# Kernel tuning notes

Measured on AMD Instinct MI355X. Metric: run time of the kernel, lower is better.

The kernel has to match this reference:

```python
import jax, jax.numpy as jnp
import numpy as np

HEADS = 8
DIM_HEAD = 64


def setup_inputs() -> dict:
    key = jax.random.key(0)
    ks = jax.random.split(key, 6)
    b, n, d = 4, 2048, 512
    inner = HEADS * DIM_HEAD  # 512
    return {
        "x": jax.random.normal(ks[0], (b, n, d), dtype=jnp.float32),
        "W_v": jax.random.normal(ks[1], (d, inner), dtype=jnp.float32) * 0.02,
        "W_sigma": jax.random.normal(ks[2], (d, HEADS), dtype=jnp.float32) * 0.02,
        "b_sigma": jax.random.normal(ks[3], (HEADS,), dtype=jnp.float32) * 0.02,
        "W_out": jax.random.normal(ks[4], (inner, d), dtype=jnp.float32) * 0.02,
        "b_out": jax.random.normal(ks[5], (d,), dtype=jnp.float32) * 0.02,
    }


def reference(x, W_v, W_sigma, b_sigma, W_out, b_out):
    b, n, d = x.shape
    h, dh = HEADS, DIM_HEAD
    # |i - j| distance matrix (linspace(1,n,n) differences == arange differences)
    pos = jnp.arange(n, dtype=x.dtype)
    dist = jnp.abs(pos[:, None] - pos[None, :])  # (n, n)
    # per-query-row sigma: (b, h, n)
    sigma = jax.nn.sigmoid(jnp.einsum("bnd,dh->bhn", x, W_sigma) + b_sigma[None, :, None])
    denom = jnp.exp(sigma) + 1.0  # (b, h, n)
    # prior[b,h,i,j] = softmax_j( -|i-j| / (exp(sigma[b,h,i]) + 1) )
    prior = jax.nn.softmax(-dist[None, None, :, :] / denom[..., None], axis=-1)  # (b,h,n,n)
    v = (x @ W_v).reshape(b, n, h, dh).transpose(0, 2, 1, 3)  # (b,h,n,dh)
    out = jnp.einsum("bhij,bhjd->bhid", prior, v)  # (b,h,n,dh)
    out = out.transpose(0, 2, 1, 3).reshape(b, n, h * dh)
    return out @ W_out + b_out
```

## Files before the change

### kernel.cpp

```cpp
#include <hip/hip_runtime.h>
#include <hip/hip_bf16.h>

#define B 4
#define N 2048
#define D 512
#define H 8
#define DH 64
#define ROWS (B * N)
#define WIN 64
#define LPAD 64
#define RPAD 128
#define SEG (LPAD + N + RPAD)
#define LDV (B * SEG)

using bf16x8 = __attribute__((ext_vector_type(8))) short;
using f32x4  = __attribute__((ext_vector_type(4))) float;
using f32x16 = __attribute__((ext_vector_type(16))) float;

static __device__ __forceinline__ unsigned short f2bf(float f) {
    unsigned u = __builtin_bit_cast(unsigned, f);
    u += 0x7fffu + ((u >> 16) & 1u);
    return (unsigned short)(u >> 16);
}
static __device__ __forceinline__ unsigned pack2(float a, float b) {
    return (unsigned)f2bf(a) | ((unsigned)f2bf(b) << 16);
}

__global__ __launch_bounds__(256) void prep_fused(const float* __restrict__ x,
                                                  const float* __restrict__ Ws,
                                                  const float* __restrict__ bs,
                                                  const float* __restrict__ Wv,
                                                  const float* __restrict__ Wo,
                                                  unsigned short* __restrict__ xbf,
                                                  float* __restrict__ l2rbuf,
                                                  unsigned short* __restrict__ WvT,
                                                  unsigned short* __restrict__ WoT,
                                                  unsigned short* __restrict__ Vt) {
    __shared__ float tile[64][65];
    const int bx = blockIdx.x;

    if (bx < 2048) {
        const int wid = threadIdx.x >> 6, lane = threadIdx.x & 63;
        const int row = bx * 4 + wid;
        const float* xr = x + (size_t)row * D + lane * 8;
        const float4 a = *reinterpret_cast<const float4*>(xr);
        const float4 c = *reinterpret_cast<const float4*>(xr + 4);
        float v[8] = {a.x, a.y, a.z, a.w, c.x, c.y, c.z, c.w};

        uint4 o;
        o.x = pack2(v[0], v[1]); o.y = pack2(v[2], v[3]);
        o.z = pack2(v[4], v[5]); o.w = pack2(v[6], v[7]);
        *reinterpret_cast<uint4*>(xbf + (size_t)row * D + lane * 8) = o;

        const float4* Ws4 = reinterpret_cast<const float4*>(Ws);
        f32x4 alo = (f32x4)0.0f, ahi = (f32x4)0.0f;
#pragma unroll
        for (int j = 0; j < 8; j++) {
            const int e = lane * 8 + j;
            const float4 wl = Ws4[e * 2], wh = Ws4[e * 2 + 1];
            alo[0] += v[j] * wl.x; alo[1] += v[j] * wl.y; alo[2] += v[j] * wl.z; alo[3] += v[j] * wl.w;
            ahi[0] += v[j] * wh.x; ahi[1] += v[j] * wh.y; ahi[2] += v[j] * wh.z; ahi[3] += v[j] * wh.w;
        }
#pragma unroll
        for (int off = 1; off < 64; off <<= 1) {
#pragma unroll
            for (int c2 = 0; c2 < 4; c2++) {
                alo[c2] += __shfl_xor(alo[c2], off, 64);
                ahi[c2] += __shfl_xor(ahi[c2], off, 64);
            }
        }
        if (lane < 8) {
            const int h = lane;
            const float acc = (h < 4) ? alo[h] : ahi[h - 4];
            const float z = acc + bs[h];
            const float sig = 1.0f / (1.0f + expf(-z));
            const float s = expf(sig) + 1.0f;
            l2rbuf[(size_t)row * H + h] = -1.4426950408889634f / s;
        }
        return;
    }

    if (bx < 2176) {
        const int idx = bx - 2048;
        const bool second = idx >= 64;
        const int id2 = idx & 63;
        const float* src = second ? Wo : Wv;
        unsigned short* dst = second ? WoT : WvT;
        const int n0 = (id2 & 7) * 64, k0 = (id2 >> 3) * 64;
        const int tr = threadIdx.x >> 4, tc = threadIdx.x & 15;
#pragma unroll
        for (int it = 0; it < 4; it++) {
            const int r = it * 16 + tr;
            const float4 v = *reinterpret_cast<const float4*>(&src[(size_t)(k0 + r) * 512 + n0 + tc * 4]);
            tile[r][tc * 4 + 0] = v.x; tile[r][tc * 4 + 1] = v.y;
            tile[r][tc * 4 + 2] = v.z; tile[r][tc * 4 + 3] = v.w;
        }
        __syncthreads();
#pragma unroll
        for (int it = 0; it < 4; it++) {
            const int r = it * 16 + tr;
            ushort4 o;
            o.x = f2bf(tile[tc * 4 + 0][r]); o.y = f2bf(tile[tc * 4 + 1][r]);
            o.z = f2bf(tile[tc * 4 + 2][r]); o.w = f2bf(tile[tc * 4 + 3][r]);
            *reinterpret_cast<ushort4*>(&dst[(size_t)(n0 + r) * 512 + k0 + tc * 4]) = o;
        }
        return;
    }

    {
        const int idx = bx - 2176;
        for (int t = idx * 256 + threadIdx.x; t < 512 * 4 * 24; t += 64 * 256) {
            const int c = t % 24;
            const int bb = (t / 24) & 3;
            const int row = t / 96;
            const int col = (c < 8) ? bb * SEG + c * 8 : bb * SEG + LPAD + N + (c - 8) * 8;
            *reinterpret_cast<uint4*>(Vt + (size_t)row * LDV + col) = uint4{0, 0, 0, 0};
        }
    }
}

#define GBK 64
#define GK  512

template <int MODE>
__global__ __launch_bounds__(256) void gemm_bf16(const unsigned short* __restrict__ A,
                                                 const unsigned short* __restrict__ Bt,
                                                 const float* __restrict__ bias,
                                                 void* __restrict__ Cout,
                                                 int ldc) {
    __shared__ unsigned short As[2][64][GBK];
    __shared__ unsigned short Bs[2][64][GBK];
    const int tid = threadIdx.x;
    const int lane = tid & 63, wid = tid >> 6;
    const int wr = wid >> 1, wc = wid & 1;
    int bm, bn;
    if (MODE == 0) {
        const int xcd = blockIdx.x & 7, idx = blockIdx.x >> 3;
        bm = xcd * 16 + (idx >> 3);
        bn = idx & 7;
    } else {
        bn = blockIdx.x; bm = blockIdx.y;
    }
    const int fr = lane & 15, kg = lane >> 4;

    f32x4 acc[2][2] = {};

    const unsigned short* Ab = A + (size_t)bm * 64 * GK;
    const unsigned short* Bb = Bt + (size_t)bn * 64 * GK;
    const int r32 = tid >> 3, c8 = (tid & 7) * 8;

    auto stage = [&](int buf, int k0) {
#pragma unroll
        for (int it = 0; it < 2; it++) {
            const unsigned short* g = Ab + (size_t)(it * 32 + r32) * GK + k0 + c8;
            __builtin_amdgcn_global_load_lds(
                (const __attribute__((address_space(1))) void*)g,
                (__attribute__((address_space(3))) void*)&As[buf][it * 32 + r32][c8], 16, 0, 0);
        }
#pragma unroll
        for (int it = 0; it < 2; it++) {
            const unsigned short* g = Bb + (size_t)(it * 32 + r32) * GK + k0 + c8;
            __builtin_amdgcn_global_load_lds(
                (const __attribute__((address_space(1))) void*)g,
                (__attribute__((address_space(3))) void*)&Bs[buf][it * 32 + r32][c8], 16, 0, 0);
        }
    };

    stage(0, 0);
    __syncthreads();
    int cur = 0;
#pragma unroll
    for (int kt = 0; kt < GK / GBK; kt++) {
        if (kt + 1 < GK / GBK) stage(cur ^ 1, (kt + 1) * GBK);
#pragma unroll
        for (int ks = 0; ks < 2; ks++) {
            bf16x8 af[2], bfr[2];
#pragma unroll
            for (int m = 0; m < 2; m++)
                af[m] = *reinterpret_cast<const bf16x8*>(&As[cur][wr * 32 + m * 16 + fr][ks * 32 + kg * 8]);
#pragma unroll
            for (int n = 0; n < 2; n++)
                bfr[n] = *reinterpret_cast<const bf16x8*>(&Bs[cur][wc * 32 + n * 16 + fr][ks * 32 + kg * 8]);
#pragma unroll
            for (int m = 0; m < 2; m++)
#pragma unroll
                for (int n = 0; n < 2; n++)
                    acc[m][n] = __builtin_amdgcn_mfma_f32_16x16x32_bf16(af[m], bfr[n], acc[m][n], 0, 0, 0);
        }
        __syncthreads();
        cur ^= 1;
    }

#pragma unroll
    for (int n = 0; n < 2; n++) {
        const int col = bn * 64 + wc * 32 + n * 16 + fr;
        const float bv = (MODE == 0 && bias) ? bias[col] : 0.0f;
        const int cp = (MODE == 2) ? ((col >> 11) * SEG + LPAD + (col & 2047)) : col;
#pragma unroll
        for (int m = 0; m < 2; m++) {
            const int row0 = bm * 64 + wr * 32 + m * 16 + kg * 4;
#pragma unroll
            for (int j = 0; j < 4; j++) {
                const int row = row0 + j;
                if (MODE == 0)
                    ((float*)Cout)[(size_t)row * ldc + col] = acc[m][n][j] + bv;
                else
                    ((unsigned short*)Cout)[(size_t)row * ldc + cp] = f2bf(acc[m][n][j]);
            }
        }
    }
}

__global__ __launch_bounds__(256) void attn_mfma(const unsigned short* __restrict__ Vt,
                                                 const float* __restrict__ l2rbuf,
                                                 unsigned short* __restrict__ O) {
    const int wid = threadIdx.x >> 6;
    const int lane = threadIdx.x & 63;
    const int il = lane & 31, hi = lane >> 5;
    const int gi = blockIdx.x * 4 + wid;
    const int iblk = gi & 63;
    const int bh = gi >> 6;
    const int h = bh & 7;
    const int b = bh >> 3;
    const int i0 = iblk * 32;

    const int i = i0 + il;
    const float l2rf = l2rbuf[((size_t)(b * N + i)) * H + h];

    const unsigned short* Va = Vt + (size_t)(h * DH + il) * LDV + (size_t)b * SEG + i0 + hi * 8;

    f32x16 acc0 = (f32x16)0.0f, acc1 = (f32x16)0.0f;
    __builtin_amdgcn_s_setprio(1);
#pragma unroll
    for (int ks = 0; ks < 10; ks++) {
        const float jb = (float)(ks * 16 + hi * 8 - WIN - il);
        float wv[8];
#pragma unroll
        for (int e = 0; e < 8; e++)
            wv[e] = __builtin_amdgcn_exp2f(l2rf * __builtin_fabsf(jb + (float)e));
        uint4 uw;
        uw.x = pack2(wv[0], wv[1]); uw.y = pack2(wv[2], wv[3]);
        uw.z = pack2(wv[4], wv[5]); uw.w = pack2(wv[6], wv[7]);
        const bf16x8 pB = __builtin_bit_cast(bf16x8, uw);
        const bf16x8 a0 = *reinterpret_cast<const bf16x8*>(Va + (size_t)ks * 16);
        const bf16x8 a1 = *reinterpret_cast<const bf16x8*>(Va + (size_t)32 * LDV + (size_t)ks * 16);
        acc0 = __builtin_amdgcn_mfma_f32_32x32x16_bf16(a0, pB, acc0, 0, 0, 0);
        acc1 = __builtin_amdgcn_mfma_f32_32x32x16_bf16(a1, pB, acc1, 0, 0, 0);
    }
    __builtin_amdgcn_s_setprio(0);

    const float rr = __builtin_amdgcn_exp2f(l2rf);
    const float inv1mr = 1.0f / (1.0f - rr);
    const float rl = __builtin_amdgcn_exp2f(l2rf * (float)(i + 1));
    const float rg = __builtin_amdgcn_exp2f(l2rf * (float)(N - i));
    const float invz = 1.0f / (1.0f + (2.0f * rr - rl - rg) * inv1mr);

    unsigned short* orow = O + ((size_t)(b * N + i)) * D + h * DH + 4 * hi;
#pragma unroll
    for (int q = 0; q < 4; q++) {
        uint2 o0, o1;
        o0.x = pack2(acc0[4 * q + 0] * invz, acc0[4 * q + 1] * invz);
        o0.y = pack2(acc0[4 * q + 2] * invz, acc0[4 * q + 3] * invz);
        *reinterpret_cast<uint2*>(orow + 8 * q) = o0;
        o1.x = pack2(acc1[4 * q + 0] * invz, acc1[4 * q + 1] * invz);
        o1.y = pack2(acc1[4 * q + 2] * invz, acc1[4 * q + 3] * invz);
        *reinterpret_cast<uint2*>(orow + 32 + 8 * q) = o1;
    }
}

extern "C" void kernel_launch(void* const* d_in, const int* in_sizes, int n_in,
                              void* d_out, int out_size, void* d_ws, size_t ws_size,
                              hipStream_t stream) {
    const float* x      = (const float*)d_in[0];
    const float* W_v    = (const float*)d_in[1];
    const float* W_sig  = (const float*)d_in[2];
    const float* b_sig  = (const float*)d_in[3];
    const float* W_out  = (const float*)d_in[4];
    const float* b_out  = (const float*)d_in[5];
    float* out = (float*)d_out;

    char* ws = (char*)d_ws;
    unsigned short* Vt   = (unsigned short*)ws;
    unsigned short* xbf  = (unsigned short*)(ws + (size_t)9  * 1024 * 1024);
    unsigned short* WvT  = (unsigned short*)(ws + (size_t)17 * 1024 * 1024);
    unsigned short* WoT  = (unsigned short*)(ws + (size_t)17 * 1024 * 1024 + 524288);
    float*          l2r  = (float*)(ws + (size_t)18 * 1024 * 1024);
    unsigned short* attnOut = xbf;

    prep_fused<<<2240, 256, 0, stream>>>(x, W_sig, b_sig, W_v, W_out,
                                         xbf, l2r, WvT, WoT, Vt);

    {
        dim3 grid(128, 8);
        gemm_bf16<2><<<grid, 256, 0, stream>>>(WvT, xbf, nullptr, Vt, LDV);
    }
    attn_mfma<<<B * H * (N / 32) / 4, 256, 0, stream>>>(Vt, l2r, attnOut);
    gemm_bf16<0><<<1024, 256, 0, stream>>>(attnOut, WoT, b_out, out, D);
}
```

Baseline: 62.79 us.

## Narrow attention window and split head dim across waves with swizzled block order

Shrinks the banded prior window from 64 to 48 on each side (8 MFMA k-steps instead of 10) and splits each 32-row tile's 64-wide head dimension across two waves, doubling the grid to 1024 blocks. Block indices are remapped so consecutive blocks are spread across XCDs. The aim is less redundant exp and MFMA work per wave and more parallelism, at the cost of recomputing the weights in both halves. Truncating the window further adds approximation error for small decay rates, though the normalizer still uses the analytic full-row sum.

```diff
diff --git a/kernel.cpp b/kernel.cpp
--- a/kernel.cpp
+++ b/kernel.cpp
@@ -8,6 +8,7 @@
 #define DH 64
 #define ROWS (B * N)
 #define WIN 64
+#define AWIN 48
 #define LPAD 64
 #define RPAD 128
 #define SEG (LPAD + N + RPAD)
@@ -217,9 +218,11 @@
     const int wid = threadIdx.x >> 6;
     const int lane = threadIdx.x & 63;
     const int il = lane & 31, hi = lane >> 5;
-    const int gi = blockIdx.x * 4 + wid;
-    const int iblk = gi & 63;
-    const int bh = gi >> 6;
+    const int sbid = (blockIdx.x & 7) * 128 + (blockIdx.x >> 3);
+    const int gi = sbid * 4 + wid;
+    const int dhalf = gi & 1;
+    const int iblk = (gi >> 1) & 63;
+    const int bh = gi >> 7;
     const int h = bh & 7;
     const int b = bh >> 3;
     const int i0 = iblk * 32;
@@ -227,13 +230,14 @@
     const int i = i0 + il;
     const float l2rf = l2rbuf[((size_t)(b * N + i)) * H + h];
 
-    const unsigned short* Va = Vt + (size_t)(h * DH + il) * LDV + (size_t)b * SEG + i0 + hi * 8;
-
-    f32x16 acc0 = (f32x16)0.0f, acc1 = (f32x16)0.0f;
+    const unsigned short* Va = Vt + (size_t)(h * DH + dhalf * 32 + il) * LDV
+                              + (size_t)b * SEG + (LPAD - AWIN) + i0 + hi * 8;
+
+    f32x16 acc = (f32x16)0.0f;
     __builtin_amdgcn_s_setprio(1);
 #pragma unroll
-    for (int ks = 0; ks < 10; ks++) {
-        const float jb = (float)(ks * 16 + hi * 8 - WIN - il);
+    for (int ks = 0; ks < 8; ks++) {
+        const float jb = (float)(ks * 16 + hi * 8 - AWIN - il);
         float wv[8];
 #pragma unroll
         for (int e = 0; e < 8; e++)
@@ -243,9 +247,7 @@
         uw.z = pack2(wv[4], wv[5]); uw.w = pack2(wv[6], wv[7]);
         const bf16x8 pB = __builtin_bit_cast(bf16x8, uw);
         const bf16x8 a0 = *reinterpret_cast<const bf16x8*>(Va + (size_t)ks * 16);
-        const bf16x8 a1 = *reinterpret_cast<const bf16x8*>(Va + (size_t)32 * LDV + (size_t)ks * 16);
-        acc0 = __builtin_amdgcn_mfma_f32_32x32x16_bf16(a0, pB, acc0, 0, 0, 0);
-        acc1 = __builtin_amdgcn_mfma_f32_32x32x16_bf16(a1, pB, acc1, 0, 0, 0);
+        acc = __builtin_amdgcn_mfma_f32_32x32x16_bf16(a0, pB, acc, 0, 0, 0);
     }
     __builtin_amdgcn_s_setprio(0);
 
@@ -255,16 +257,13 @@
     const float rg = __builtin_amdgcn_exp2f(l2rf * (float)(N - i));
     const float invz = 1.0f / (1.0f + (2.0f * rr - rl - rg) * inv1mr);
 
-    unsigned short* orow = O + ((size_t)(b * N + i)) * D + h * DH + 4 * hi;
+    unsigned short* orow = O + ((size_t)(b * N + i)) * D + h * DH + dhalf * 32 + 4 * hi;
 #pragma unroll
     for (int q = 0; q < 4; q++) {
-        uint2 o0, o1;
-        o0.x = pack2(acc0[4 * q + 0] * invz, acc0[4 * q + 1] * invz);
-        o0.y = pack2(acc0[4 * q + 2] * invz, acc0[4 * q + 3] * invz);
+        uint2 o0;
+        o0.x = pack2(acc[4 * q + 0] * invz, acc[4 * q + 1] * invz);
+        o0.y = pack2(acc[4 * q + 2] * invz, acc[4 * q + 3] * invz);
         *reinterpret_cast<uint2*>(orow + 8 * q) = o0;
-        o1.x = pack2(acc1[4 * q + 0] * invz, acc1[4 * q + 1] * invz);
-        o1.y = pack2(acc1[4 * q + 2] * invz, acc1[4 * q + 3] * invz);
-        *reinterpret_cast<uint2*>(orow + 32 + 8 * q) = o1;
     }
 }
 
@@ -294,6 +293,6 @@
         dim3 grid(128, 8);
         gemm_bf16<2><<<grid, 256, 0, stream>>>(WvT, xbf, nullptr, Vt, LDV);
     }
-    attn_mfma<<<B * H * (N / 32) / 4, 256, 0, stream>>>(Vt, l2r, attnOut);
+    attn_mfma<<<1024, 256, 0, stream>>>(Vt, l2r, attnOut);
     gemm_bf16<0><<<1024, 256, 0, stream>>>(attnOut, WoT, b_out, out, D);
 }
```

Result: no change. 61.67 us (-1.8%).
